# Kernel tuning notes

Hardware: AMD Instinct MI355X
Metric: run time of the kernel (lower is better)

## Reference

```python
import jax, jax.numpy as jnp
import numpy as np

TAU = 0.1


def setup_inputs() -> dict:
    key = jax.random.key(0)
    k1, k2, k3 = jax.random.split(key, 3)
    B, C, H, W = 32, 1, 512, 512
    input1 = jax.random.normal(k1, (B, C, H, W), dtype=jnp.float32)
    input2 = jax.random.normal(k2, (B, C, H, W), dtype=jnp.float32)
    mask = jax.random.uniform(k3, (B, C, H, W), dtype=jnp.float32)
    return {"input1": input1, "input2": input2, "mask": mask}


def reference(input1, input2, mask):
    # logit=True: apply sigmoid first
    x1 = jax.nn.sigmoid(input1)
    x2 = jax.nn.sigmoid(input2)
    B = x1.shape[0]
    N = x1.shape[1] * x1.shape[2] * x1.shape[3]

    # positive similarity: masked MSE per sample over (C,H,W)
    sim_pos = jnp.exp(-jnp.mean((mask * (x1 - x2)) ** 2, axis=(1, 2, 3)) / TAU)

    # negative similarities: all-pairs MSE via GEMM expansion trick
    # mean((a-b)^2) = (|a|^2 + |b|^2 - 2 a.b) / N
    f1 = x1.reshape(B, N)
    f2 = x2.reshape(B, N)
    sq1 = jnp.sum(f1 * f1, axis=1)  # [B]
    sq2 = jnp.sum(f2 * f2, axis=1)  # [B]
    cross = f1 @ f2.T               # [B,B]
    d = (sq1[:, None] + sq2[None, :] - 2.0 * cross) / N
    sim = jnp.exp(-d / TAU)         # [B,B]
    # exclude b1 == b2 diagonal terms
    sim_neg = jnp.sum(sim, axis=1) - jnp.diagonal(sim)

    loss = -jnp.log(sim_pos / (sim_pos + sim_neg))
    return jnp.mean(loss)
```

## Files before the change

kernel.cpp:

```cpp
#include <hip/hip_runtime.h>
#include <hip/hip_bf16.h>

#define NF 262144
#define NROWS 32

typedef __attribute__((ext_vector_type(8))) __bf16 bf16x8;
typedef __attribute__((ext_vector_type(16))) float f32x16;

__device__ __forceinline__ float sigmoid_fast(float x) {
    float e = __expf(-x);
    return __builtin_amdgcn_rcpf(1.0f + e);
}

__global__ __launch_bounds__(256) void cl_main(const float* __restrict__ in1,
                                               const float* __restrict__ in2,
                                               const float* __restrict__ msk,
                                               float* __restrict__ ws) {
    const int tid  = threadIdx.x;
    const int wid  = tid >> 6;
    const int lane = tid & 63;
    const int r    = lane & 31;
    const int g    = lane >> 5;
    const int gw   = blockIdx.x * 4 + wid;
    const size_t rowoff = (size_t)r * NF;
    const int cbase = gw * 128 + g * 8;

    f32x16 acc;
    #pragma unroll
    for (int k = 0; k < 16; ++k) acc[k] = 0.0f;
    float pos = 0.0f, q1 = 0.0f, q2 = 0.0f;

    #pragma unroll 2
    for (int s = 0; s < 8; ++s) {
        const int c0 = cbase + s * 16;
        float xa[8], xb[8], xm[8];
        const float4* p1 = reinterpret_cast<const float4*>(in1 + rowoff + c0);
        const float4* p2 = reinterpret_cast<const float4*>(in2 + rowoff + c0);
        const float4* pm = reinterpret_cast<const float4*>(msk + rowoff + c0);
        *reinterpret_cast<float4*>(&xa[0]) = p1[0];
        *reinterpret_cast<float4*>(&xa[4]) = p1[1];
        *reinterpret_cast<float4*>(&xb[0]) = p2[0];
        *reinterpret_cast<float4*>(&xb[4]) = p2[1];
        *reinterpret_cast<float4*>(&xm[0]) = pm[0];
        *reinterpret_cast<float4*>(&xm[4]) = pm[1];

        bf16x8 fa, fb;
        #pragma unroll
        for (int e = 0; e < 8; ++e) {
            float sa = sigmoid_fast(xa[e]);
            float sb = sigmoid_fast(xb[e]);
            float t = xm[e] * (sa - sb);
            pos = fmaf(t, t, pos);
            q1  = fmaf(sa, sa, q1);
            q2  = fmaf(sb, sb, q2);
            fa[e] = (__bf16)sa;
            fb[e] = (__bf16)sb;
        }
        acc = __builtin_amdgcn_mfma_f32_32x32x16_bf16(fa, fb, acc, 0, 0, 0);
    }

    __shared__ float s_cross[32][32];
    __shared__ float s_vec[3][32];
    for (int idx = tid; idx < 1024; idx += 256) (&s_cross[0][0])[idx] = 0.0f;
    if (tid < 96) (&s_vec[0][0])[tid] = 0.0f;
    __syncthreads();

    pos += __shfl_down(pos, 32);
    q1  += __shfl_down(q1, 32);
    q2  += __shfl_down(q2, 32);
    if (lane < 32) {
        atomicAdd(&s_vec[0][r], pos);
        atomicAdd(&s_vec[1][r], q1);
        atomicAdd(&s_vec[2][r], q2);
    }
    const int col = lane & 31;
    const int rhi = (lane >> 5) * 4;
    #pragma unroll
    for (int reg = 0; reg < 16; ++reg) {
        const int row = (reg & 3) + 8 * (reg >> 2) + rhi;
        atomicAdd(&s_cross[row][col], acc[reg]);
    }
    __syncthreads();

    for (int idx = tid; idx < 1024; idx += 256) atomicAdd(&ws[idx], (&s_cross[0][0])[idx]);
    if (tid < 96) atomicAdd(&ws[1024 + tid], (&s_vec[0][0])[tid]);
}

__global__ __launch_bounds__(1024) void cl_final(const float* __restrict__ ws,
                                                 float* __restrict__ out) {
    __shared__ float s_loss[32];
    const int tid = threadIdx.x;
    const int i = tid >> 5, j = tid & 31;
    const float invN = 1.0f / (float)NF;

    float c  = ws[i * 32 + j];
    float p  = ws[1024 + i];
    float s1 = ws[1056 + i];
    float s2 = ws[1088 + j];

    float d = (s1 + s2 - 2.0f * c) * invN;
    float sim = (i == j) ? 0.0f : expf(-d * 10.0f);
    #pragma unroll
    for (int off = 16; off; off >>= 1) sim += __shfl_xor(sim, off);

    if (j == 0) {
        float sp = expf(-p * invN * 10.0f);
        s_loss[i] = -logf(sp / (sp + sim));
    }
    __syncthreads();
    if (tid == 0) {
        float t = 0.0f;
        #pragma unroll
        for (int k = 0; k < 32; ++k) t += s_loss[k];
        out[0] = t * (1.0f / 32.0f);
    }
}

extern "C" void kernel_launch(void* const* d_in, const int* in_sizes, int n_in,
                              void* d_out, int out_size, void* d_ws, size_t ws_size,
                              hipStream_t stream) {
    const float* in1 = (const float*)d_in[0];
    const float* in2 = (const float*)d_in[1];
    const float* msk = (const float*)d_in[2];
    float* out = (float*)d_out;
    float* ws  = (float*)d_ws;

    hipMemsetAsync(ws, 0, 1120 * sizeof(float), stream);
    cl_main<<<512, 256, 0, stream>>>(in1, in2, msk, ws);
    cl_final<<<1, 1024, 0, stream>>>(ws, out);
}
```

Baseline: 51.31 us.

## Quadruple grid size and spread global atomics across workspace slices

Each wave now handles 32 columns instead of 128, so the grid grows from 512 to 2048 blocks for more parallelism and latency hiding. To keep the larger number of global atomic adds from all landing on one 1120-float region, blocks write into up to 64 replicated slices selected by block index, and the final kernel sums the slices. This trades more atomics and shared-memory reduction work per byte loaded, plus a larger memset and a serial slice loop in the final kernel, for less atomic contention and better occupancy.

```diff
diff --git a/kernel.cpp b/kernel.cpp
--- a/kernel.cpp
+++ b/kernel.cpp
@@ -3,6 +3,7 @@
 
 #define NF 262144
 #define NROWS 32
+#define SLICE 1120
 
 typedef __attribute__((ext_vector_type(8))) __bf16 bf16x8;
 typedef __attribute__((ext_vector_type(16))) float f32x16;
@@ -15,7 +16,8 @@
 __global__ __launch_bounds__(256) void cl_main(const float* __restrict__ in1,
                                                const float* __restrict__ in2,
                                                const float* __restrict__ msk,
-                                               float* __restrict__ ws) {
+                                               float* __restrict__ ws,
+                                               int kmask) {
     const int tid  = threadIdx.x;
     const int wid  = tid >> 6;
     const int lane = tid & 63;
@@ -23,15 +25,15 @@
     const int g    = lane >> 5;
     const int gw   = blockIdx.x * 4 + wid;
     const size_t rowoff = (size_t)r * NF;
-    const int cbase = gw * 128 + g * 8;
+    const int cbase = gw * 32 + g * 8;
 
     f32x16 acc;
     #pragma unroll
     for (int k = 0; k < 16; ++k) acc[k] = 0.0f;
     float pos = 0.0f, q1 = 0.0f, q2 = 0.0f;
 
-    #pragma unroll 2
-    for (int s = 0; s < 8; ++s) {
+    #pragma unroll
+    for (int s = 0; s < 2; ++s) {
         const int c0 = cbase + s * 16;
         float xa[8], xb[8], xm[8];
         const float4* p1 = reinterpret_cast<const float4*>(in1 + rowoff + c0);
@@ -82,21 +84,27 @@
     }
     __syncthreads();
 
-    for (int idx = tid; idx < 1024; idx += 256) atomicAdd(&ws[idx], (&s_cross[0][0])[idx]);
-    if (tid < 96) atomicAdd(&ws[1024 + tid], (&s_vec[0][0])[tid]);
+    float* slice = ws + (size_t)(blockIdx.x & kmask) * SLICE;
+    for (int idx = tid; idx < 1024; idx += 256) atomicAdd(&slice[idx], (&s_cross[0][0])[idx]);
+    if (tid < 96) atomicAdd(&slice[1024 + tid], (&s_vec[0][0])[tid]);
 }
 
 __global__ __launch_bounds__(1024) void cl_final(const float* __restrict__ ws,
-                                                 float* __restrict__ out) {
+                                                 float* __restrict__ out,
+                                                 int nslices) {
     __shared__ float s_loss[32];
     const int tid = threadIdx.x;
     const int i = tid >> 5, j = tid & 31;
     const float invN = 1.0f / (float)NF;
 
-    float c  = ws[i * 32 + j];
-    float p  = ws[1024 + i];
-    float s1 = ws[1056 + i];
-    float s2 = ws[1088 + j];
+    float c = 0.0f, p = 0.0f, s1 = 0.0f, s2 = 0.0f;
+    for (int k = 0; k < nslices; ++k) {
+        const float* sl = ws + (size_t)k * SLICE;
+        c  += sl[i * 32 + j];
+        p  += sl[1024 + i];
+        s1 += sl[1056 + i];
+        s2 += sl[1088 + j];
+    }
 
     float d = (s1 + s2 - 2.0f * c) * invN;
     float sim = (i == j) ? 0.0f : expf(-d * 10.0f);
@@ -125,7 +133,11 @@
     float* out = (float*)d_out;
     float* ws  = (float*)d_ws;
 
-    hipMemsetAsync(ws, 0, 1120 * sizeof(float), stream);
-    cl_main<<<512, 256, 0, stream>>>(in1, in2, msk, ws);
-    cl_final<<<1, 1024, 0, stream>>>(ws, out);
+    int kcap = (int)(ws_size / (SLICE * sizeof(float)));
+    int K = 1;
+    while (K * 2 <= kcap && K < 64) K *= 2;
+
+    hipMemsetAsync(ws, 0, (size_t)K * SLICE * sizeof(float), stream);
+    cl_main<<<2048, 256, 0, stream>>>(in1, in2, msk, ws, K - 1);
+    cl_final<<<1, 1024, 0, stream>>>(ws, out, K);
 }
```

Result: slower. 81.23 us (+58.3%).

## Split fused kernel into pack, LDS-staged GEMM, and tree reduction

Applied to the files above, without the earlier changes.

Replaces the single fused sigmoid+MFMA kernel with a pack kernel that writes sigmoid outputs as a bf16 panel in MFMA-friendly record layout. A GEMM kernel then streams that panel into swizzled LDS via async global-to-LDS loads with double buffering, and per-block partials are reduced without atomics. The aim is to remove global atomic contention and strided row loads. In exchange it adds an extra round trip of the bf16 panel through global memory and two more kernel launches.

```diff
diff --git a/kernel.cpp b/kernel.cpp
--- a/kernel.cpp
+++ b/kernel.cpp
@@ -3,8 +3,19 @@
 
 #define NF 262144
 #define NROWS 32
+#define CHUNK 8192
+#define RECB 8192
+#define NREC 4096
+#define CSTRIDE 1088
+#define NKG 16
+
+#define PANEL_OFF 0
+#define CREC_OFF  8388608
+#define WS2_OFF   (CREC_OFF + 1024 * CSTRIDE)
+#define PQ_OFF    (WS2_OFF + NKG * CSTRIDE)
 
 typedef __attribute__((ext_vector_type(8))) __bf16 bf16x8;
+typedef __attribute__((ext_vector_type(4))) __bf16 bf16x4;
 typedef __attribute__((ext_vector_type(16))) float f32x16;
 
 __device__ __forceinline__ float sigmoid_fast(float x) {
@@ -12,78 +23,150 @@
     return __builtin_amdgcn_rcpf(1.0f + e);
 }
 
-__global__ __launch_bounds__(256) void cl_main(const float* __restrict__ in1,
+__device__ __forceinline__ void gload16(const void* g, const float* l) {
+    __builtin_amdgcn_global_load_lds(
+        (const __attribute__((address_space(1))) void*)g,
+        (__attribute__((address_space(3))) void*)l, 16, 0, 0);
+}
+
+__global__ __launch_bounds__(256) void cl_pack(const float* __restrict__ in1,
                                                const float* __restrict__ in2,
                                                const float* __restrict__ msk,
                                                float* __restrict__ ws) {
     const int tid  = threadIdx.x;
-    const int wid  = tid >> 6;
+    const int r    = blockIdx.x >> 5;
+    const int c    = blockIdx.x & 31;
+    const int sub  = tid >> 4;
+    const int slot = tid & 15;
+
+    const size_t base = (size_t)r * NF + (size_t)c * CHUNK;
+    const float* p1 = in1 + base;
+    const float* p2 = in2 + base;
+    const float* pm = msk + base;
+    char* panel = (char*)(ws + PANEL_OFF);
+
+    float pos = 0.0f, q1 = 0.0f, q2 = 0.0f;
+
+    #pragma unroll
+    for (int i = 0; i < 8; ++i) {
+        const int kt  = i * 16 + sub;
+        const int off = kt * 64 + slot * 4;
+        float4 a = *(const float4*)(p1 + off);
+        float4 b = *(const float4*)(p2 + off);
+        float4 m = *(const float4*)(pm + off);
+
+        bf16x4 ua, ub;
+        #pragma unroll
+        for (int e = 0; e < 4; ++e) {
+            float xa = (e == 0) ? a.x : (e == 1) ? a.y : (e == 2) ? a.z : a.w;
+            float xb = (e == 0) ? b.x : (e == 1) ? b.y : (e == 2) ? b.z : b.w;
+            float xm = (e == 0) ? m.x : (e == 1) ? m.y : (e == 2) ? m.z : m.w;
+            float sa = sigmoid_fast(xa);
+            float sb = sigmoid_fast(xb);
+            float d  = xm * (sa - sb);
+            pos = fmaf(d, d, pos);
+            q1  = fmaf(sa, sa, q1);
+            q2  = fmaf(sb, sb, q2);
+            ua[e] = (__bf16)sa;
+            ub[e] = (__bf16)sb;
+        }
+        const int K = c * 128 + kt;
+        char* rec = panel + (size_t)K * RECB + r * 128 + slot * 8;
+        *(bf16x4*)rec          = ua;
+        *(bf16x4*)(rec + 4096) = ub;
+    }
+
+    __shared__ float sred[4][3];
+    #pragma unroll
+    for (int off = 32; off; off >>= 1) {
+        pos += __shfl_xor(pos, off);
+        q1  += __shfl_xor(q1, off);
+        q2  += __shfl_xor(q2, off);
+    }
+    if ((tid & 63) == 0) {
+        sred[tid >> 6][0] = pos; sred[tid >> 6][1] = q1; sred[tid >> 6][2] = q2;
+    }
+    __syncthreads();
+    if (tid == 0) {
+        float* PQ = ws + PQ_OFF + c * 96;
+        PQ[r]      = sred[0][0] + sred[1][0] + sred[2][0] + sred[3][0];
+        PQ[32 + r] = sred[0][1] + sred[1][1] + sred[2][1] + sred[3][1];
+        PQ[64 + r] = sred[0][2] + sred[1][2] + sred[2][2] + sred[3][2];
+    }
+}
+
+__global__ __launch_bounds__(256) void cl_gemm(const float* __restrict__ ws_ro,
+                                               float* __restrict__ ws) {
+    __shared__ float smem[4096];
+
+    const int tid  = threadIdx.x;
+    const int w    = tid >> 6;
     const int lane = tid & 63;
     const int r    = lane & 31;
     const int g    = lane >> 5;
-    const int gw   = blockIdx.x * 4 + wid;
-    const size_t rowoff = (size_t)r * NF;
-    const int cbase = gw * 128 + g * 8;
+
+    const char* panel = (const char*)(ws_ro + PANEL_OFF);
+    const int rec0 = blockIdx.x * 4;
 
     f32x16 acc;
     #pragma unroll
     for (int k = 0; k < 16; ++k) acc[k] = 0.0f;
-    float pos = 0.0f, q1 = 0.0f, q2 = 0.0f;
-
-    #pragma unroll 2
-    for (int s = 0; s < 8; ++s) {
-        const int c0 = cbase + s * 16;
-        float xa[8], xb[8], xm[8];
-        const float4* p1 = reinterpret_cast<const float4*>(in1 + rowoff + c0);
-        const float4* p2 = reinterpret_cast<const float4*>(in2 + rowoff + c0);
-        const float4* pm = reinterpret_cast<const float4*>(msk + rowoff + c0);
-        *reinterpret_cast<float4*>(&xa[0]) = p1[0];
-        *reinterpret_cast<float4*>(&xa[4]) = p1[1];
-        *reinterpret_cast<float4*>(&xb[0]) = p2[0];
-        *reinterpret_cast<float4*>(&xb[4]) = p2[1];
-        *reinterpret_cast<float4*>(&xm[0]) = pm[0];
-        *reinterpret_cast<float4*>(&xm[4]) = pm[1];
-
-        bf16x8 fa, fb;
+
+    auto stage = [&](int p, int rec) {
+        const char* recb = panel + (size_t)rec * RECB;
         #pragma unroll
-        for (int e = 0; e < 8; ++e) {
-            float sa = sigmoid_fast(xa[e]);
-            float sb = sigmoid_fast(xb[e]);
-            float t = xm[e] * (sa - sb);
-            pos = fmaf(t, t, pos);
-            q1  = fmaf(sa, sa, q1);
-            q2  = fmaf(sb, sb, q2);
-            fa[e] = (__bf16)sa;
-            fb[e] = (__bf16)sb;
+        for (int m = 0; m < 2; ++m) {
+            const int n   = w * 2 + m;
+            const int a   = n >> 2;
+            const int row = (n & 3) * 8 + (lane >> 3);
+            const int sc  = (lane & 7) ^ (row & 7);
+            gload16(recb + a * 4096 + row * 128 + sc * 16,
+                    smem + p * 2048 + n * 256);
         }
+    };
+
+    auto compute = [&](int p) {
+        const int cs = (w * 2 + g) ^ (r & 7);
+        const float* base = smem + p * 2048 + r * 32 + cs * 4;
+        bf16x8 fa = *(const bf16x8*)(base);
+        bf16x8 fb = *(const bf16x8*)(base + 1024);
         acc = __builtin_amdgcn_mfma_f32_32x32x16_bf16(fa, fb, acc, 0, 0, 0);
-    }
-
-    __shared__ float s_cross[32][32];
-    __shared__ float s_vec[3][32];
-    for (int idx = tid; idx < 1024; idx += 256) (&s_cross[0][0])[idx] = 0.0f;
-    if (tid < 96) (&s_vec[0][0])[tid] = 0.0f;
-    __syncthreads();
-
-    pos += __shfl_down(pos, 32);
-    q1  += __shfl_down(q1, 32);
-    q2  += __shfl_down(q2, 32);
-    if (lane < 32) {
-        atomicAdd(&s_vec[0][r], pos);
-        atomicAdd(&s_vec[1][r], q1);
-        atomicAdd(&s_vec[2][r], q2);
-    }
+    };
+
+    stage(0, rec0);
+    __syncthreads();
+    #pragma unroll
+    for (int t = 0; t < 3; ++t) {
+        stage((t + 1) & 1, rec0 + t + 1);
+        compute(t & 1);
+        __syncthreads();
+    }
+    compute(1);
+    __syncthreads();
+
     const int col = lane & 31;
     const int rhi = (lane >> 5) * 4;
     #pragma unroll
     for (int reg = 0; reg < 16; ++reg) {
         const int row = (reg & 3) + 8 * (reg >> 2) + rhi;
-        atomicAdd(&s_cross[row][col], acc[reg]);
-    }
-    __syncthreads();
-
-    for (int idx = tid; idx < 1024; idx += 256) atomicAdd(&ws[idx], (&s_cross[0][0])[idx]);
-    if (tid < 96) atomicAdd(&ws[1024 + tid], (&s_vec[0][0])[tid]);
+        smem[w * 1024 + row * 32 + col] = acc[reg];
+    }
+    __syncthreads();
+
+    float* P = ws + CREC_OFF + (size_t)blockIdx.x * CSTRIDE;
+    for (int idx = tid; idx < 1024; idx += 256)
+        P[idx] = smem[idx] + smem[1024 + idx] + smem[2048 + idx] + smem[3072 + idx];
+}
+
+__global__ __launch_bounds__(256) void cl_reduce(const float* __restrict__ ws_ro,
+                                                 float* __restrict__ ws) {
+    const int kg   = blockIdx.x >> 2;
+    const int slot = (blockIdx.x & 3) * 256 + threadIdx.x;
+    const float* base = ws_ro + CREC_OFF + (size_t)kg * 64 * CSTRIDE + slot;
+    float s = 0.0f;
+    #pragma unroll 8
+    for (int k = 0; k < 64; ++k) s += base[(size_t)k * CSTRIDE];
+    ws[WS2_OFF + kg * CSTRIDE + slot] = s;
 }
 
 __global__ __launch_bounds__(1024) void cl_final(const float* __restrict__ ws,
@@ -93,10 +176,17 @@
     const int i = tid >> 5, j = tid & 31;
     const float invN = 1.0f / (float)NF;
 
-    float c  = ws[i * 32 + j];
-    float p  = ws[1024 + i];
-    float s1 = ws[1056 + i];
-    float s2 = ws[1088 + j];
+    float c = 0.0f, p = 0.0f, s1 = 0.0f, s2 = 0.0f;
+    #pragma unroll
+    for (int k = 0; k < NKG; ++k)
+        c += ws[WS2_OFF + (size_t)k * CSTRIDE + i * 32 + j];
+    #pragma unroll
+    for (int ch = 0; ch < 32; ++ch) {
+        const float* PQ = ws + PQ_OFF + ch * 96;
+        p  += PQ[i];
+        s1 += PQ[32 + i];
+        s2 += PQ[64 + j];
+    }
 
     float d = (s1 + s2 - 2.0f * c) * invN;
     float sim = (i == j) ? 0.0f : expf(-d * 10.0f);
@@ -125,7 +215,8 @@
     float* out = (float*)d_out;
     float* ws  = (float*)d_ws;
 
-    hipMemsetAsync(ws, 0, 1120 * sizeof(float), stream);
-    cl_main<<<512, 256, 0, stream>>>(in1, in2, msk, ws);
-    cl_final<<<1, 1024, 0, stream>>>(ws, out);
-}
+    cl_pack  <<<1024, 256, 0, stream>>>(in1, in2, msk, ws);
+    cl_gemm  <<<1024, 256, 0, stream>>>(ws, ws);
+    cl_reduce<<<64,   256, 0, stream>>>(ws, ws);
+    cl_final <<<1,   1024, 0, stream>>>(ws, out);
+}
```

Result: faster. 45.10 us (-12.1%).
